# Performance work log

Measured on AMD Instinct MI355X. Metric: run time of the kernel, lower is better.

Reference implementation:

```python
import jax, jax.numpy as jnp
import numpy as np

N_EMBD = 1024
N_HEAD = 16
B, T = 8, 1024
EPS = 1e-5


def setup_inputs() -> dict:
    key = jax.random.key(0)
    ks = jax.random.split(key, 12)
    C = N_EMBD
    s_in = 1.0 / np.sqrt(C)
    s_ff = 1.0 / np.sqrt(4 * C)
    inp = {
        "x": jax.random.normal(ks[0], (B, T, C), dtype=jnp.float32),
        "mask": jnp.tril(jnp.ones((T, T), dtype=jnp.int32))[None, None, :, :],
        "ln1_w": jnp.ones((C,), jnp.float32),
        "ln1_b": jnp.zeros((C,), jnp.float32),
        "ln2_w": jnp.ones((C,), jnp.float32),
        "ln2_b": jnp.zeros((C,), jnp.float32),
        "wq": jax.random.normal(ks[1], (C, C), jnp.float32) * s_in,
        "bq": jnp.zeros((C,), jnp.float32),
        "wk": jax.random.normal(ks[2], (C, C), jnp.float32) * s_in,
        "bk": jnp.zeros((C,), jnp.float32),
        "wv": jax.random.normal(ks[3], (C, C), jnp.float32) * s_in,
        "bv": jnp.zeros((C,), jnp.float32),
        "wo": jax.random.normal(ks[4], (C, C), jnp.float32) * s_in,
        "bo": jnp.zeros((C,), jnp.float32),
        "w1": jax.random.normal(ks[5], (C, 4 * C), jnp.float32) * s_in,
        "b1": jnp.zeros((4 * C,), jnp.float32),
        "w2": jax.random.normal(ks[6], (4 * C, C), jnp.float32) * s_ff,
        "b2": jnp.zeros((C,), jnp.float32),
    }
    return inp


def _layer_norm(x, w, b):
    mu = jnp.mean(x, axis=-1, keepdims=True)
    var = jnp.mean(jnp.square(x - mu), axis=-1, keepdims=True)
    return (x - mu) * jax.lax.rsqrt(var + EPS) * w + b


def reference(x, mask, ln1_w, ln1_b, ln2_w, ln2_b,
              wq, bq, wk, bk, wv, bv, wo, bo, w1, b1, w2, b2):
    Bx, Tx, C = x.shape
    H = N_HEAD
    d = C // H
    h = _layer_norm(x, ln1_w, ln1_b)
    q = (h @ wq + bq).reshape(Bx, Tx, H, d)
    k = (h @ wk + bk).reshape(Bx, Tx, H, d)
    v = (h @ wv + bv).reshape(Bx, Tx, H, d)
    # [B,H,Tq,Tk] scores, scaled by sqrt(head_dim)
    scores = jnp.einsum('bqhd,bkhd->bhqk', q, k) / jnp.sqrt(jnp.float32(d))
    scores = jnp.where(mask == 0, -jnp.inf, scores)
    attn = jax.nn.softmax(scores, axis=-1)
    ctx = jnp.einsum('bhqk,bkhd->bqhd', attn, v).reshape(Bx, Tx, C)
    x = x + (ctx @ wo + bo)
    h2 = _layer_norm(x, ln2_w, ln2_b)
    ff = jax.nn.gelu(h2 @ w1 + b1, approximate=False) @ w2 + b2
    return x + ff
```

## Files before the change

kernel.cpp:

```cpp
#include <hip/hip_runtime.h>
#include <hip/hip_bf16.h>
#include <math.h>


#define DEVI __device__ __forceinline__

typedef __attribute__((ext_vector_type(4))) float floatx4;
typedef __attribute__((ext_vector_type(8))) short shortx8;

DEVI ushort f2b(float f) {
    __hip_bfloat16 h = __float2bfloat16(f);
    return __builtin_bit_cast(ushort, h);
}

DEVI void gl_lds16(const ushort* g, ushort* l) {
    __builtin_amdgcn_global_load_lds(
        (const __attribute__((address_space(1))) void*)g,
        (__attribute__((address_space(3))) void*)l, 16, 0, 0);
}

__global__ void transp_kernel(const float* __restrict__ src,
                              ushort* __restrict__ dst, int R, int C) {
    __shared__ float tile[32][33];
    const int c0 = blockIdx.x * 32, r0 = blockIdx.y * 32;
    const int tx = threadIdx.x, ty = threadIdx.y;
#pragma unroll
    for (int i = 0; i < 32; i += 8)
        tile[ty + i][tx] = src[(size_t)(r0 + ty + i) * C + c0 + tx];
    __syncthreads();
#pragma unroll
    for (int i = 0; i < 32; i += 8)
        dst[(size_t)(c0 + ty + i) * R + r0 + tx] = f2b(tile[tx][ty + i]);
}

__global__ __launch_bounds__(256)
void ln_kernel(const float* __restrict__ x, const float* __restrict__ w,
               const float* __restrict__ b, ushort* __restrict__ out) {
    __shared__ float red[8];
    const int m = blockIdx.x;
    const int tid = threadIdx.x;
    const float4 xv = *(const float4*)&x[(size_t)m * 1024 + tid * 4];
    float s  = xv.x + xv.y + xv.z + xv.w;
    float s2 = xv.x * xv.x + xv.y * xv.y + xv.z * xv.z + xv.w * xv.w;
#pragma unroll
    for (int o = 32; o >= 1; o >>= 1) {
        s  += __shfl_xor(s, o, 64);
        s2 += __shfl_xor(s2, o, 64);
    }
    const int wv_ = tid >> 6;
    if ((tid & 63) == 0) { red[wv_] = s; red[4 + wv_] = s2; }
    __syncthreads();
    s  = red[0] + red[1] + red[2] + red[3];
    s2 = red[4] + red[5] + red[6] + red[7];
    const float mu   = s * (1.0f / 1024.0f);
    const float var  = s2 * (1.0f / 1024.0f) - mu * mu;
    const float rstd = rsqrtf(var + 1e-5f);
    const float4 wv = *(const float4*)&w[tid * 4];
    const float4 bv = *(const float4*)&b[tid * 4];
    ushort o4[4];
    o4[0] = f2b((xv.x - mu) * rstd * wv.x + bv.x);
    o4[1] = f2b((xv.y - mu) * rstd * wv.y + bv.y);
    o4[2] = f2b((xv.z - mu) * rstd * wv.z + bv.z);
    o4[3] = f2b((xv.w - mu) * rstd * wv.w + bv.w);
    *(uint2*)&out[(size_t)m * 1024 + tid * 4] = *(uint2*)o4;
}

template <int MODE>
__global__ __launch_bounds__(256)
void gemm_bt(const ushort* __restrict__ A, const ushort* __restrict__ Bt,
             const float* __restrict__ bias, void* __restrict__ out,
             const float* __restrict__ resid, int M, int N, int K,
             void* __restrict__ out2, void* __restrict__ out3) {
    __shared__ ushort sA[128 * 64];
    __shared__ ushort sB[128 * 64];
    const int tid  = threadIdx.x;
    const int lane = tid & 63;
    const int wave = tid >> 6;
    const int quad = lane >> 4;
    const int l15  = lane & 15;
    const int wm   = (wave & 1) * 64;
    const int wn   = (wave >> 1) * 64;
    const int m0   = blockIdx.y * 128;
    const int n0   = blockIdx.x * 128;

    floatx4 acc[4][4] = {};

    const int lrow = lane >> 3;
    const int scb  = (lane & 7) ^ lrow;
    const ushort* Ag = A  + (size_t)(m0 + wave * 8 + lrow) * K + scb * 8;
    const ushort* Bg = Bt + (size_t)(n0 + wave * 8 + lrow) * K + scb * 8;

    for (int k0 = 0; k0 < K; k0 += 64) {
        __syncthreads();
#pragma unroll
        for (int p = 0; p < 4; ++p) {
            gl_lds16(Ag + (size_t)(p * 32) * K + k0, sA + (p * 32 + wave * 8) * 64);
            gl_lds16(Bg + (size_t)(p * 32) * K + k0, sB + (p * 32 + wave * 8) * 64);
        }
        __syncthreads();
#pragma unroll
        for (int ks = 0; ks < 2; ++ks) {
            shortx8 af[4], bf[4];
#pragma unroll
            for (int i = 0; i < 4; ++i) {
                const int r = wm + i * 16 + l15;
                const int c = (ks * 4 + quad) ^ (r & 7);
                af[i] = *(const shortx8*)&sA[r * 64 + c * 8];
            }
#pragma unroll
            for (int j = 0; j < 4; ++j) {
                const int r = wn + j * 16 + l15;
                const int c = (ks * 4 + quad) ^ (r & 7);
                bf[j] = *(const shortx8*)&sB[r * 64 + c * 8];
            }
#pragma unroll
            for (int i = 0; i < 4; ++i)
#pragma unroll
                for (int j = 0; j < 4; ++j)
                    acc[i][j] = __builtin_amdgcn_mfma_f32_16x16x32_bf16(
                        af[i], bf[j], acc[i][j], 0, 0, 0);
        }
    }
#pragma unroll
    for (int i = 0; i < 4; ++i) {
#pragma unroll
        for (int j = 0; j < 4; ++j) {
#pragma unroll
            for (int r = 0; r < 4; ++r) {
                const int gm = m0 + wm + i * 16 + quad * 4 + r;
                const int gn = n0 + wn + j * 16 + l15;
                float v = acc[i][j][r] + bias[gn];
                if constexpr (MODE == 1) {
                    const int mat = gn >> 10;
                    const int cn  = gn & 1023;
                    const int h = cn >> 6, dd = cn & 63;
                    const int bb = gm >> 10, t = gm & 1023;
                    const size_t bh = (size_t)(bb * 16 + h);
                    const ushort val = f2b(v);
                    if (mat == 0)
                        ((ushort*)out )[(bh * 1024 + t) * 64 + dd] = val;
                    else if (mat == 1)
                        ((ushort*)out2)[(bh * 1024 + t) * 64 + dd] = val;
                    else
                        ((ushort*)out3)[(bh * 64 + dd) * 1024 + t] = val;
                } else if constexpr (MODE == 2) {
                    v += resid[(size_t)gm * N + gn];
                    ((float*)out)[(size_t)gm * N + gn] = v;
                } else if constexpr (MODE == 3) {
                    const float g = 0.5f * v * (1.0f + erff(v * 0.70710678f));
                    ((ushort*)out)[(size_t)gm * N + gn] = f2b(g);
                }
            }
        }
    }
}

__global__ __launch_bounds__(256)
void attn_kernel(const ushort* __restrict__ Q, const ushort* __restrict__ Kk,
                 const ushort* __restrict__ Vt, ushort* __restrict__ ctx) {
    __shared__ ushort sK[64 * 64];
    __shared__ ushort sV[64 * 64];
    __shared__ ushort sP[4][16 * 72];

    const int tid  = threadIdx.x;
    const int lane = tid & 63;
    const int wave = tid >> 6;
    const int quad = lane >> 4;
    const int l15  = lane & 15;

    const int qb = 15 - (blockIdx.x >> 7);
    const int bh = blockIdx.x & 127;
    const size_t base = (size_t)bh << 16;
    const int bb = bh >> 4, h = bh & 15;

    const int lrow = lane >> 3;
    const int scb  = (lane & 7) ^ lrow;
    const ushort* Kg = Kk + base + (size_t)(wave * 8 + lrow) * 64 + scb * 8;
    const ushort* Vg = Vt + base + (size_t)(wave * 8 + lrow) * 1024 + scb * 8;

    const int qrow = qb * 64 + wave * 16 + l15;
    const shortx8 qf0 = *(const shortx8*)&Q[base + (size_t)qrow * 64 + quad * 8];
    const shortx8 qf1 = *(const shortx8*)&Q[base + (size_t)qrow * 64 + 32 + quad * 8];

    const float SC = 0.125f * 1.44269504f;

    float mstate[4], lstate[4];
    floatx4 oacc[4] = {};
#pragma unroll
    for (int r = 0; r < 4; ++r) { mstate[r] = -__builtin_inff(); lstate[r] = 0.0f; }

    for (int kt = 0; kt <= qb; ++kt) {
        __syncthreads();
#pragma unroll
        for (int p = 0; p < 2; ++p) {
            gl_lds16(Kg + (size_t)kt * 4096 + (size_t)p * 2048,
                     sK + (p * 32 + wave * 8) * 64);
            gl_lds16(Vg + (size_t)kt * 64 + (size_t)p * 32 * 1024,
                     sV + (p * 32 + wave * 8) * 64);
        }
        __syncthreads();

        floatx4 s[4];
#pragma unroll
        for (int nt = 0; nt < 4; ++nt) {
            const int r = nt * 16 + l15;
            const int c0 = quad ^ (r & 7);
            const int c1 = (4 + quad) ^ (r & 7);
            const shortx8 kf0 = *(const shortx8*)&sK[r * 64 + c0 * 8];
            const shortx8 kf1 = *(const shortx8*)&sK[r * 64 + c1 * 8];
            floatx4 z = {};
            z = __builtin_amdgcn_mfma_f32_16x16x32_bf16(qf0, kf0, z, 0, 0, 0);
            z = __builtin_amdgcn_mfma_f32_16x16x32_bf16(qf1, kf1, z, 0, 0, 0);
            s[nt] = z;
        }
#pragma unroll
        for (int nt = 0; nt < 4; ++nt)
#pragma unroll
            for (int r = 0; r < 4; ++r) {
                float sv = s[nt][r] * SC;
                if (kt == qb) {
                    const int col = nt * 16 + l15;
                    const int row = wave * 16 + quad * 4 + r;
                    if (col > row) sv = -__builtin_inff();
                }
                s[nt][r] = sv;
            }
        float mnew[4], alpha[4];
#pragma unroll
        for (int r = 0; r < 4; ++r) {
            float mt = fmaxf(fmaxf(s[0][r], s[1][r]), fmaxf(s[2][r], s[3][r]));
#pragma unroll
            for (int o = 8; o >= 1; o >>= 1) mt = fmaxf(mt, __shfl_xor(mt, o, 64));
            mnew[r]  = fmaxf(mstate[r], mt);
            alpha[r] = exp2f(mstate[r] - mnew[r]);
            mstate[r] = mnew[r];
        }
#pragma unroll
        for (int r = 0; r < 4; ++r) {
            float rs = 0.0f;
#pragma unroll
            for (int nt = 0; nt < 4; ++nt) {
                const float p = exp2f(s[nt][r] - mnew[r]);
                s[nt][r] = p;
                rs += p;
            }
#pragma unroll
            for (int o = 8; o >= 1; o >>= 1) rs += __shfl_xor(rs, o, 64);
            lstate[r] = alpha[r] * lstate[r] + rs;
#pragma unroll
            for (int dt = 0; dt < 4; ++dt) oacc[dt][r] *= alpha[r];
        }
#pragma unroll
        for (int nt = 0; nt < 4; ++nt)
#pragma unroll
            for (int r = 0; r < 4; ++r)
                sP[wave][(quad * 4 + r) * 72 + nt * 16 + l15] = f2b(s[nt][r]);
        __asm__ volatile("s_waitcnt lgkmcnt(0)" ::: "memory");
        const shortx8 pf0 = *(const shortx8*)&sP[wave][l15 * 72 + quad * 8];
        const shortx8 pf1 = *(const shortx8*)&sP[wave][l15 * 72 + 32 + quad * 8];
#pragma unroll
        for (int dt = 0; dt < 4; ++dt) {
            const int r = dt * 16 + l15;
            const int c0 = quad ^ (r & 7);
            const int c1 = (4 + quad) ^ (r & 7);
            const shortx8 v0 = *(const shortx8*)&sV[r * 64 + c0 * 8];
            const shortx8 v1 = *(const shortx8*)&sV[r * 64 + c1 * 8];
            oacc[dt] = __builtin_amdgcn_mfma_f32_16x16x32_bf16(pf0, v0, oacc[dt], 0, 0, 0);
            oacc[dt] = __builtin_amdgcn_mfma_f32_16x16x32_bf16(pf1, v1, oacc[dt], 0, 0, 0);
        }
    }
#pragma unroll
    for (int dt = 0; dt < 4; ++dt)
#pragma unroll
        for (int r = 0; r < 4; ++r) {
            const int t = qb * 64 + wave * 16 + quad * 4 + r;
            const int dim = dt * 16 + l15;
            const float v = oacc[dt][r] / lstate[r];
            ctx[(size_t)(bb * 1024 + t) * 1024 + h * 64 + dim] = f2b(v);
        }
}

extern "C" void kernel_launch(void* const* d_in, const int* in_sizes, int n_in,
                              void* d_out, int out_size, void* d_ws, size_t ws_size,
                              hipStream_t stream) {
    const float* x    = (const float*)d_in[0];
    const float* ln1w = (const float*)d_in[2];
    const float* ln1b = (const float*)d_in[3];
    const float* ln2w = (const float*)d_in[4];
    const float* ln2b = (const float*)d_in[5];
    const float* wq   = (const float*)d_in[6];
    const float* bq   = (const float*)d_in[7];
    const float* wk   = (const float*)d_in[8];
    const float* bk   = (const float*)d_in[9];
    const float* wv   = (const float*)d_in[10];
    const float* bv   = (const float*)d_in[11];
    const float* wo   = (const float*)d_in[12];
    const float* bo   = (const float*)d_in[13];
    const float* w1   = (const float*)d_in[14];
    const float* b1   = (const float*)d_in[15];
    const float* w2   = (const float*)d_in[16];
    const float* b2   = (const float*)d_in[17];

    char* ws = (char*)d_ws;
    const size_t MB = 1024 * 1024;
    ushort* WQKVT = (ushort*)(ws + 0 * MB);
    ushort* WOT   = (ushort*)(ws + 6 * MB);
    ushort* W1T   = (ushort*)(ws + 8 * MB);
    ushort* W2T   = (ushort*)(ws + 16 * MB);
    ushort* H1    = (ushort*)(ws + 24 * MB);
    ushort* H2    = H1;
    ushort* Qb    = (ushort*)(ws + 40 * MB);
    ushort* Kb    = (ushort*)(ws + 56 * MB);
    ushort* Vbt   = (ushort*)(ws + 72 * MB);
    ushort* FF1   = (ushort*)(ws + 40 * MB);
    ushort* CTX   = (ushort*)(ws + 104 * MB);

    float* xout = (float*)d_out;

    float* bqkv = (float*)(ws + 120 * MB);
    hipMemcpyAsync(bqkv,        bq, 1024 * 4, hipMemcpyDeviceToDevice, stream);
    hipMemcpyAsync(bqkv + 1024, bk, 1024 * 4, hipMemcpyDeviceToDevice, stream);
    hipMemcpyAsync(bqkv + 2048, bv, 1024 * 4, hipMemcpyDeviceToDevice, stream);

    const dim3 tb(32, 8);
    transp_kernel<<<dim3(32, 32), tb, 0, stream>>>(wq, WQKVT, 1024, 1024);
    transp_kernel<<<dim3(32, 32), tb, 0, stream>>>(wk, WQKVT + 1024 * 1024, 1024, 1024);
    transp_kernel<<<dim3(32, 32), tb, 0, stream>>>(wv, WQKVT + 2048 * 1024, 1024, 1024);
    transp_kernel<<<dim3(32, 32), tb, 0, stream>>>(wo, WOT, 1024, 1024);
    transp_kernel<<<dim3(128, 32), tb, 0, stream>>>(w1, W1T, 1024, 4096);
    transp_kernel<<<dim3(32, 128), tb, 0, stream>>>(w2, W2T, 4096, 1024);

    ln_kernel<<<8192, 256, 0, stream>>>(x, ln1w, ln1b, H1);

    gemm_bt<1><<<dim3(24, 64), 256, 0, stream>>>(H1, WQKVT, bqkv, Qb, nullptr,
                                                 8192, 3072, 1024, Kb, Vbt);

    attn_kernel<<<2048, 256, 0, stream>>>(Qb, Kb, Vbt, CTX);

    gemm_bt<2><<<dim3(8, 64), 256, 0, stream>>>(CTX, WOT, bo, xout, x,
                                                8192, 1024, 1024, nullptr, nullptr);

    ln_kernel<<<8192, 256, 0, stream>>>(xout, ln2w, ln2b, H2);

    gemm_bt<3><<<dim3(32, 64), 256, 0, stream>>>(H2, W1T, b1, FF1, nullptr,
                                                 8192, 4096, 1024, nullptr, nullptr);

    gemm_bt<2><<<dim3(8, 64), 256, 0, stream>>>(FF1, W2T, b2, xout, xout,
                                                8192, 1024, 4096, nullptr, nullptr);

    (void)in_sizes; (void)n_in; (void)out_size; (void)ws_size;
}
```

Baseline: 543.8 us.

## Switch GEMMs to 32x32 MFMA, tanh GELU, LDS-staged V transpose, merge prep launches

Replaces the 16x16x32 bf16 MFMA tiles with 32x32x16 tiles in the shared GEMM, which halves the count of LDS fragment loads per MFMA. Replaces the erf GELU with an exp2-based tanh approximation. Stages the transposed V output through LDS so it is written as coalesced 16-byte stores, and picks the Q/K/V bias pointer per block. It also fuses the four square weight transposes into one launch and drops the three bias memcpys. The tanh GELU changes numerics relative to the exact erf reference.

```diff
diff --git a/kernel.cpp b/kernel.cpp
--- a/kernel.cpp
+++ b/kernel.cpp
@@ -6,6 +6,7 @@
 #define DEVI __device__ __forceinline__
 
 typedef __attribute__((ext_vector_type(4))) float floatx4;
+typedef __attribute__((ext_vector_type(16))) float floatx16;
 typedef __attribute__((ext_vector_type(8))) short shortx8;
 
 DEVI ushort f2b(float f) {
@@ -17,6 +18,33 @@
     __builtin_amdgcn_global_load_lds(
         (const __attribute__((address_space(1))) void*)g,
         (__attribute__((address_space(3))) void*)l, 16, 0, 0);
+}
+
+DEVI float gelu_f(float v) {
+    const float u0 = 0.7978845608f * v * (1.0f + 0.044715f * v * v);
+    const float u  = fminf(fmaxf(u0, -15.0f), 15.0f);
+    const float e  = exp2f(u * 2.885390082f);
+    const float th = 1.0f - 2.0f / (e + 1.0f);
+    return 0.5f * v * (1.0f + th);
+}
+
+__global__ void transp4_kernel(const float* __restrict__ s0, const float* __restrict__ s1,
+                               const float* __restrict__ s2, const float* __restrict__ s3,
+                               ushort* __restrict__ d0, ushort* __restrict__ d1,
+                               ushort* __restrict__ d2, ushort* __restrict__ d3) {
+    const int z = blockIdx.z;
+    const float* src = (z == 0) ? s0 : (z == 1) ? s1 : (z == 2) ? s2 : s3;
+    ushort*      dst = (z == 0) ? d0 : (z == 1) ? d1 : (z == 2) ? d2 : d3;
+    __shared__ float tile[32][33];
+    const int c0 = blockIdx.x * 32, r0 = blockIdx.y * 32;
+    const int tx = threadIdx.x, ty = threadIdx.y;
+#pragma unroll
+    for (int i = 0; i < 32; i += 8)
+        tile[ty + i][tx] = src[(size_t)(r0 + ty + i) * 1024 + c0 + tx];
+    __syncthreads();
+#pragma unroll
+    for (int i = 0; i < 32; i += 8)
+        dst[(size_t)(c0 + ty + i) * 1024 + r0 + tx] = f2b(tile[tx][ty + i]);
 }
 
 __global__ void transp_kernel(const float* __restrict__ src,
@@ -68,22 +96,26 @@
 template <int MODE>
 __global__ __launch_bounds__(256)
 void gemm_bt(const ushort* __restrict__ A, const ushort* __restrict__ Bt,
-             const float* __restrict__ bias, void* __restrict__ out,
-             const float* __restrict__ resid, int M, int N, int K,
-             void* __restrict__ out2, void* __restrict__ out3) {
-    __shared__ ushort sA[128 * 64];
-    __shared__ ushort sB[128 * 64];
+             const float* __restrict__ biasQ, const float* __restrict__ biasK,
+             const float* __restrict__ biasV,
+             void* __restrict__ out, void* __restrict__ out2, void* __restrict__ out3,
+             const float* __restrict__ resid, int M, int N, int K) {
+    constexpr int LDSN = (MODE == 1) ? (128 * 144) : (128 * 64 * 2);
+    __shared__ ushort lds[LDSN];
+    ushort* sA = lds;
+    ushort* sB = lds + 128 * 64;
+
     const int tid  = threadIdx.x;
     const int lane = tid & 63;
     const int wave = tid >> 6;
-    const int quad = lane >> 4;
-    const int l15  = lane & 15;
+    const int l31  = lane & 31;
+    const int half = lane >> 5;
     const int wm   = (wave & 1) * 64;
     const int wn   = (wave >> 1) * 64;
     const int m0   = blockIdx.y * 128;
     const int n0   = blockIdx.x * 128;
 
-    floatx4 acc[4][4] = {};
+    floatx16 acc[2][2] = {};
 
     const int lrow = lane >> 3;
     const int scb  = (lane & 7) ^ lrow;
@@ -99,60 +131,101 @@
         }
         __syncthreads();
 #pragma unroll
-        for (int ks = 0; ks < 2; ++ks) {
-            shortx8 af[4], bf[4];
-#pragma unroll
-            for (int i = 0; i < 4; ++i) {
-                const int r = wm + i * 16 + l15;
-                const int c = (ks * 4 + quad) ^ (r & 7);
-                af[i] = *(const shortx8*)&sA[r * 64 + c * 8];
-            }
-#pragma unroll
-            for (int j = 0; j < 4; ++j) {
-                const int r = wn + j * 16 + l15;
-                const int c = (ks * 4 + quad) ^ (r & 7);
-                bf[j] = *(const shortx8*)&sB[r * 64 + c * 8];
-            }
-#pragma unroll
-            for (int i = 0; i < 4; ++i)
-#pragma unroll
-                for (int j = 0; j < 4; ++j)
-                    acc[i][j] = __builtin_amdgcn_mfma_f32_16x16x32_bf16(
+        for (int ks = 0; ks < 4; ++ks) {
+            const int cx = ks * 2 + half;
+            shortx8 af[2], bf[2];
+#pragma unroll
+            for (int i = 0; i < 2; ++i) {
+                const int r = wm + i * 32 + l31;
+                af[i] = *(const shortx8*)&sA[r * 64 + (cx ^ (r & 7)) * 8];
+            }
+#pragma unroll
+            for (int j = 0; j < 2; ++j) {
+                const int r = wn + j * 32 + l31;
+                bf[j] = *(const shortx8*)&sB[r * 64 + (cx ^ (r & 7)) * 8];
+            }
+#pragma unroll
+            for (int i = 0; i < 2; ++i)
+#pragma unroll
+                for (int j = 0; j < 2; ++j)
+                    acc[i][j] = __builtin_amdgcn_mfma_f32_32x32x16_bf16(
                         af[i], bf[j], acc[i][j], 0, 0, 0);
         }
     }
-#pragma unroll
-    for (int i = 0; i < 4; ++i) {
-#pragma unroll
-        for (int j = 0; j < 4; ++j) {
-#pragma unroll
-            for (int r = 0; r < 4; ++r) {
-                const int gm = m0 + wm + i * 16 + quad * 4 + r;
-                const int gn = n0 + wn + j * 16 + l15;
-                float v = acc[i][j][r] + bias[gn];
-                if constexpr (MODE == 1) {
-                    const int mat = gn >> 10;
-                    const int cn  = gn & 1023;
+
+    if constexpr (MODE == 1) {
+        const int mat = n0 >> 10;
+        if (mat < 2) {
+            const float* bp = (mat == 0) ? biasQ : biasK;
+            ushort* dst = (mat == 0) ? (ushort*)out : (ushort*)out2;
+#pragma unroll
+            for (int i = 0; i < 2; ++i)
+#pragma unroll
+                for (int j = 0; j < 2; ++j) {
+                    const int cn = (n0 & 1023) + wn + j * 32 + l31;
+                    const float bv = bp[cn];
                     const int h = cn >> 6, dd = cn & 63;
-                    const int bb = gm >> 10, t = gm & 1023;
-                    const size_t bh = (size_t)(bb * 16 + h);
-                    const ushort val = f2b(v);
-                    if (mat == 0)
-                        ((ushort*)out )[(bh * 1024 + t) * 64 + dd] = val;
-                    else if (mat == 1)
-                        ((ushort*)out2)[(bh * 1024 + t) * 64 + dd] = val;
-                    else
-                        ((ushort*)out3)[(bh * 64 + dd) * 1024 + t] = val;
-                } else if constexpr (MODE == 2) {
-                    v += resid[(size_t)gm * N + gn];
-                    ((float*)out)[(size_t)gm * N + gn] = v;
-                } else if constexpr (MODE == 3) {
-                    const float g = 0.5f * v * (1.0f + erff(v * 0.70710678f));
-                    ((ushort*)out)[(size_t)gm * N + gn] = f2b(g);
+#pragma unroll
+                    for (int reg = 0; reg < 16; ++reg) {
+                        const int gm = m0 + wm + i * 32 + (reg & 3) + 8 * (reg >> 2) + 4 * half;
+                        const int bb = gm >> 10, t = gm & 1023;
+                        dst[((size_t)(bb * 16 + h) * 1024 + t) * 64 + dd] =
+                            f2b(acc[i][j][reg] + bv);
+                    }
                 }
-            }
-        }
+        } else {
+            __syncthreads();
+            ushort* T = lds;
+#pragma unroll
+            for (int i = 0; i < 2; ++i)
+#pragma unroll
+                for (int j = 0; j < 2; ++j) {
+                    const int trow = wn + j * 32 + l31;
+                    const float bv = biasV[(n0 & 1023) + trow];
+#pragma unroll
+                    for (int rq = 0; rq < 4; ++rq) {
+                        const int tcol = wm + i * 32 + 8 * rq + 4 * half;
+                        ushort pk[4];
+#pragma unroll
+                        for (int e = 0; e < 4; ++e)
+                            pk[e] = f2b(acc[i][j][rq * 4 + e] + bv);
+                        *(uint2*)&T[trow * 144 + tcol] = *(uint2*)pk;
+                    }
+                }
+            __syncthreads();
+            const int bb = m0 >> 10;
+#pragma unroll
+            for (int pass = 0; pass < 8; ++pass) {
+                const int row = pass * 16 + (tid >> 4);
+                const int cb  = (tid & 15) * 8;
+                const uint4 val = *(const uint4*)&T[row * 144 + cb];
+                const int dd = (n0 - 2048) + row;
+                const int h = dd >> 6, dl = dd & 63;
+                const int t = (m0 & 1023) + cb;
+                *(uint4*)&((ushort*)out3)[((size_t)(bb * 16 + h) * 64 + dl) * 1024 + t] = val;
+            }
+        }
+    } else {
+#pragma unroll
+        for (int i = 0; i < 2; ++i)
+#pragma unroll
+            for (int j = 0; j < 2; ++j) {
+                const int gn = n0 + wn + j * 32 + l31;
+                const float bv = biasQ[gn];
+#pragma unroll
+                for (int reg = 0; reg < 16; ++reg) {
+                    const int gm = m0 + wm + i * 32 + (reg & 3) + 8 * (reg >> 2) + 4 * half;
+                    float v = acc[i][j][reg] + bv;
+                    if constexpr (MODE == 2) {
+                        v += resid[(size_t)gm * N + gn];
+                        ((float*)out)[(size_t)gm * N + gn] = v;
+                    } else {
+                        ((ushort*)out)[(size_t)gm * N + gn] = f2b(gelu_f(v));
+                    }
+                }
+            }
     }
+    (void)resid; (void)M;
 }
 
 __global__ __launch_bounds__(256)
@@ -317,36 +390,34 @@
 
     float* xout = (float*)d_out;
 
-    float* bqkv = (float*)(ws + 120 * MB);
-    hipMemcpyAsync(bqkv,        bq, 1024 * 4, hipMemcpyDeviceToDevice, stream);
-    hipMemcpyAsync(bqkv + 1024, bk, 1024 * 4, hipMemcpyDeviceToDevice, stream);
-    hipMemcpyAsync(bqkv + 2048, bv, 1024 * 4, hipMemcpyDeviceToDevice, stream);
-
     const dim3 tb(32, 8);
-    transp_kernel<<<dim3(32, 32), tb, 0, stream>>>(wq, WQKVT, 1024, 1024);
-    transp_kernel<<<dim3(32, 32), tb, 0, stream>>>(wk, WQKVT + 1024 * 1024, 1024, 1024);
-    transp_kernel<<<dim3(32, 32), tb, 0, stream>>>(wv, WQKVT + 2048 * 1024, 1024, 1024);
-    transp_kernel<<<dim3(32, 32), tb, 0, stream>>>(wo, WOT, 1024, 1024);
+    transp4_kernel<<<dim3(32, 32, 4), tb, 0, stream>>>(
+        wq, wk, wv, wo,
+        WQKVT, WQKVT + 1024 * 1024, WQKVT + 2048 * 1024, WOT);
     transp_kernel<<<dim3(128, 32), tb, 0, stream>>>(w1, W1T, 1024, 4096);
     transp_kernel<<<dim3(32, 128), tb, 0, stream>>>(w2, W2T, 4096, 1024);
 
     ln_kernel<<<8192, 256, 0, stream>>>(x, ln1w, ln1b, H1);
 
-    gemm_bt<1><<<dim3(24, 64), 256, 0, stream>>>(H1, WQKVT, bqkv, Qb, nullptr,
-                                                 8192, 3072, 1024, Kb, Vbt);
+    gemm_bt<1><<<dim3(24, 64), 256, 0, stream>>>(H1, WQKVT, bq, bk, bv,
+                                                 Qb, Kb, Vbt, nullptr,
+                                                 8192, 3072, 1024);
 
     attn_kernel<<<2048, 256, 0, stream>>>(Qb, Kb, Vbt, CTX);
 
-    gemm_bt<2><<<dim3(8, 64), 256, 0, stream>>>(CTX, WOT, bo, xout, x,
-                                                8192, 1024, 1024, nullptr, nullptr);
+    gemm_bt<2><<<dim3(8, 64), 256, 0, stream>>>(CTX, WOT, bo, nullptr, nullptr,
+                                                xout, nullptr, nullptr, x,
+                                                8192, 1024, 1024);
 
     ln_kernel<<<8192, 256, 0, stream>>>(xout, ln2w, ln2b, H2);
 
-    gemm_bt<3><<<dim3(32, 64), 256, 0, stream>>>(H2, W1T, b1, FF1, nullptr,
-                                                 8192, 4096, 1024, nullptr, nullptr);
-
-    gemm_bt<2><<<dim3(8, 64), 256, 0, stream>>>(FF1, W2T, b2, xout, xout,
-                                                8192, 1024, 4096, nullptr, nullptr);
+    gemm_bt<3><<<dim3(32, 64), 256, 0, stream>>>(H2, W1T, b1, nullptr, nullptr,
+                                                 FF1, nullptr, nullptr, nullptr,
+                                                 8192, 4096, 1024);
+
+    gemm_bt<2><<<dim3(8, 64), 256, 0, stream>>>(FF1, W2T, b2, nullptr, nullptr,
+                                                xout, nullptr, nullptr, xout,
+                                                8192, 1024, 4096);
 
     (void)in_sizes; (void)n_in; (void)out_size; (void)ws_size;
 }
```

After: 517.3 us. 4.9% less time.
